# Performance work log

Measured on AMD Instinct MI355X. Metric: run time of the kernel, lower is better.

## Reference

```python
import jax, jax.numpy as jnp
import numpy as np

HEADS = 16
DIM_HEAD = 64
SCALE = DIM_HEAD ** -0.5
NEG = -jnp.finfo(jnp.float32).max


def setup_inputs() -> dict:
    key = jax.random.key(0)
    ks = jax.random.split(key, 5)
    b, n, dim = 2, 2048, 1024
    inner = HEADS * DIM_HEAD
    s = dim ** -0.5  # keep pre-softmax logits well-scaled
    return {
        "x": jax.random.normal(ks[0], (b, n, dim), jnp.float32),
        "mask": jnp.ones((b, n), dtype=bool),
        "Wq": jax.random.normal(ks[1], (dim, inner), jnp.float32) * s,
        "Wk": jax.random.normal(ks[2], (dim, inner), jnp.float32) * s,
        "Wv": jax.random.normal(ks[3], (dim, inner), jnp.float32) * s,
        "Wo": jax.random.normal(ks[4], (inner, dim), jnp.float32) * s,
    }


def reference(x, mask, Wq, Wk, Wv, Wo):
    b, n, _ = x.shape
    # projections, split heads: b n (h d) -> b h n d
    def split(t):
        return t.reshape(b, n, HEADS, DIM_HEAD).transpose(0, 2, 1, 3)
    q = split(x @ Wq)
    k = split(x @ Wk)
    v = split(x @ Wv)
    dots = jnp.einsum("bhid,bhjd->bhij", q, k) * SCALE  # [b,h,n,n]
    # padding mask: b j -> b 1 1 j
    dots = jnp.where(mask[:, None, None, :], dots, NEG)
    # causal mask (strict upper triangle masked)
    causal = jnp.triu(jnp.ones((n, n), dtype=bool), k=1)
    dots = jnp.where(causal, NEG, dots)
    attn = jax.nn.softmax(dots, axis=-1)
    out = jnp.einsum("bhij,bhjd->bhid", attn, v)
    out = out.transpose(0, 2, 1, 3).reshape(b, n, HEADS * DIM_HEAD)
    return out @ Wo
```

## Files before the change

kernel.cpp:

```cpp
#include <hip/hip_runtime.h>
#include <hip/hip_bf16.h>

typedef __bf16 bf16x8 __attribute__((ext_vector_type(8)));
typedef float f32x4 __attribute__((ext_vector_type(4)));
typedef unsigned short u16;
typedef unsigned int u32;

#define MFMA16(A, B, C) __builtin_amdgcn_mfma_f32_16x16x32_bf16((A), (B), (C), 0, 0, 0)

#define BATCH 2
#define SEQ   2048
#define DIM   1024
#define NHEAD 16
#define DHEAD 64
#define MROWS 4096
#define Q_SCALE 0.18033688f

__device__ __forceinline__ u16 f2bf(float f) {
    unsigned int u = __float_as_uint(f);
    u += 0x7fff + ((u >> 16) & 1);
    return (u16)(u >> 16);
}

__device__ __forceinline__ u32 pk2bf(float a, float b) {
    __hip_bfloat162 c = __float22bfloat162_rn(float2{a, b});
    u32 r;
    __builtin_memcpy(&r, &c, 4);
    return r;
}

__device__ __forceinline__ void glds16(const u16* g, u16* l) {
    __builtin_amdgcn_global_load_lds(
        (const __attribute__((address_space(1))) u32*)g,
        (__attribute__((address_space(3))) u32*)l, 16, 0, 0);
}

__global__ __launch_bounds__(256) void prep(const float* __restrict__ x,
                                            const float* __restrict__ wq,
                                            const float* __restrict__ wk,
                                            const float* __restrict__ wv,
                                            const float* __restrict__ wo,
                                            u16* __restrict__ xb,
                                            u16* __restrict__ wt) {
    const int b = blockIdx.x;
    const int t = threadIdx.x;
    if (b < 2048) {
        int i = (b * 256 + t) * 8;
        float4 a = *(const float4*)(x + i);
        float4 c = *(const float4*)(x + i + 4);
        u16 o[8] = {f2bf(a.x), f2bf(a.y), f2bf(a.z), f2bf(a.w),
                    f2bf(c.x), f2bf(c.y), f2bf(c.z), f2bf(c.w)};
        *(uint4*)(xb + i) = *(uint4*)o;
        return;
    }
    __shared__ u16 tile[64][65];
    const int bb = b - 2048;
    const int z = bb >> 8, rem = bb & 255;
    const float* W = (z == 0) ? wq : (z == 1) ? wk : (z == 2) ? wv : wo;
    u16* out = wt + (size_t)z * DIM * DIM;
    int k0 = (rem & 15) * 64;
    int n0 = (rem >> 4) * 64;
    int c = t & 63, r4 = t >> 6;
#pragma unroll
    for (int i = 0; i < 16; i++) {
        int row = i * 4 + r4;
        tile[row][c] = f2bf(W[(size_t)(k0 + row) * DIM + n0 + c]);
    }
    __syncthreads();
#pragma unroll
    for (int i = 0; i < 16; i++) {
        int row = i * 4 + r4;
        out[(size_t)(n0 + row) * DIM + k0 + c] = tile[c][row];
    }
}

__global__ __launch_bounds__(256) void gemm_qkv(const u16* __restrict__ xb,
                                                const u16* __restrict__ wt,
                                                u16* __restrict__ qb,
                                                u16* __restrict__ kb,
                                                u16* __restrict__ vtb) {
    __shared__ __align__(16) u16 SMEM[17408];
    u16* const As = SMEM;
    u16* const Bs = SMEM + 8192;

    const int z = blockIdx.z;
    const u16* Apan = xb;
    const u16* Bpan = wt + (size_t)z * DIM * DIM;
    const int m0 = blockIdx.y * 128, n0 = blockIdx.x * 128;
    const int t = threadIdx.x, w = t >> 6, lane = t & 63;
    const int quad = lane >> 4, l16 = lane & 15;
    const int wm = (w >> 1) * 64, wn = (w & 1) * 64;
    const int srow = lane >> 3;
    const int scol = ((lane & 7) ^ srow) * 8;
    const int fo0 = ((quad) ^ (l16 & 7)) * 8;
    const int fo1 = ((4 + quad) ^ (l16 & 7)) * 8;

    f32x4 acc[4][4] = {};
    for (int k0 = 0; k0 < DIM; k0 += 64) {
        if (k0) __syncthreads();
#pragma unroll
        for (int j = 0; j < 4; j++) {
            int rb = w * 32 + j * 8;
            glds16(Apan + (size_t)(m0 + rb + srow) * DIM + k0 + scol, &As[rb * 64]);
            glds16(Bpan + (size_t)(n0 + rb + srow) * DIM + k0 + scol, &Bs[rb * 64]);
        }
        __syncthreads();

        bf16x8 af[4][2], bfr[4][2];
#pragma unroll
        for (int mt = 0; mt < 4; mt++) {
            const u16* p = &As[(wm + mt * 16 + l16) * 64];
            af[mt][0] = *(const bf16x8*)(p + fo0);
            af[mt][1] = *(const bf16x8*)(p + fo1);
        }
#pragma unroll
        for (int nt = 0; nt < 4; nt++) {
            const u16* p = &Bs[(wn + nt * 16 + l16) * 64];
            bfr[nt][0] = *(const bf16x8*)(p + fo0);
            bfr[nt][1] = *(const bf16x8*)(p + fo1);
        }
#pragma unroll
        for (int mt = 0; mt < 4; mt++)
#pragma unroll
            for (int nt = 0; nt < 4; nt++) {
                acc[mt][nt] = MFMA16(af[mt][0], bfr[nt][0], acc[mt][nt]);
                acc[mt][nt] = MFMA16(af[mt][1], bfr[nt][1], acc[mt][nt]);
            }
    }

    const int bi = m0 >> 11;
    if (z < 2) {
        const float sc = (z == 0) ? Q_SCALE : 1.0f;
        u16* dst = (z == 0) ? qb : kb;
#pragma unroll
        for (int mt = 0; mt < 4; mt++)
#pragma unroll
            for (int nt = 0; nt < 4; nt++)
#pragma unroll
                for (int r = 0; r < 4; r++) {
                    int gm = m0 + wm + mt * 16 + quad * 4 + r;
                    int gc = n0 + wn + nt * 16 + l16;
                    int si = gm & (SEQ - 1);
                    int h = gc >> 6, d = gc & 63;
                    dst[(((size_t)bi * NHEAD + h) * SEQ + si) * DHEAD + d] =
                        f2bf(acc[mt][nt][r] * sc);
                }
    } else {
        __syncthreads();
        u16* T = SMEM;
#pragma unroll
        for (int mt = 0; mt < 4; mt++)
#pragma unroll
            for (int nt = 0; nt < 4; nt++)
#pragma unroll
                for (int r = 0; r < 4; r++)
                    T[(wn + nt * 16 + l16) * 136 + wm + mt * 16 + quad * 4 + r] =
                        f2bf(acc[mt][nt][r]);
        __syncthreads();
        const int row = t >> 1;
        const int half = (t & 1) * 64;
        const int gc = n0 + row;
        const int h = gc >> 6, d = gc & 63;
        const size_t gb = (((size_t)bi * NHEAD + h) * DHEAD + d) * SEQ +
                          (m0 & (SEQ - 1)) + half;
#pragma unroll
        for (int i = 0; i < 8; i++)
            *(uint4*)&vtb[gb + i * 8] = *(const uint4*)&T[row * 136 + half + i * 8];
    }
}

#define LPAD 72
#define OSTR 68
__global__ __launch_bounds__(256) void attn(const u16* __restrict__ qg,
                                            const u16* __restrict__ kg,
                                            const u16* __restrict__ vtg,
                                            u16* __restrict__ og) {
    __shared__ __align__(16) u16 Ks[2][64 * LPAD];
    __shared__ __align__(16) u16 Vs[2][64 * LPAD];
    __shared__ __align__(16) u16 Ps[64 * LPAD];
    float* const Os = (float*)&Ks[0][0];
    float* const Ls = Os + 64 * OSTR;

    const int linear = blockIdx.x;
    const int cls = linear & 7;
    const int inner = linear >> 3;
    const int qt = 31 - (inner >> 2);
    const int bh = cls * 4 + (inner & 3);
    const int t = threadIdx.x, w = t >> 6, lane = t & 63;
    const int quad = lane >> 4, l16 = lane & 15;
    const int wq32 = (w >> 1) * 32, kh = w & 1, kh32 = kh * 32;
    const int srow = t >> 2, sc16 = (t & 3) * 16;
    const size_t qkbase = (size_t)bh * SEQ;
    const size_t vbase = (size_t)bh * DHEAD;
    const int bi = bh >> 4, hh = bh & 15;

    uint4 pk0, pk1, pv0, pv1;
    auto prefetch = [&](int j0) {
        const u16* kp = &kg[(qkbase + j0 + srow) * DHEAD + sc16];
        pk0 = *(const uint4*)kp;
        pk1 = *(const uint4*)(kp + 8);
        const u16* vp = &vtg[(vbase + srow) * SEQ + j0 + sc16];
        pv0 = *(const uint4*)vp;
        pv1 = *(const uint4*)(vp + 8);
    };

    const int q0 = qt * 64;
    const int rowmin = q0 + wq32;

    bf16x8 bq[2][2];
#pragma unroll
    for (int ct = 0; ct < 2; ct++) {
        const u16* qp = qg + (qkbase + q0 + wq32 + ct * 16 + l16) * DHEAD;
        bq[ct][0] = *(const bf16x8*)(qp + quad * 8);
        bq[ct][1] = *(const bf16x8*)(qp + 32 + quad * 8);
    }

    f32x4 accO[4][2] = {};
    float l_part[2] = {0.f, 0.f};

    prefetch(0);

    for (int jt = 0; jt <= qt; jt++) {
        const int buf = jt & 1;
        u16* ksb = &Ks[buf][0];
        u16* vsb = &Vs[buf][0];
        *(uint4*)&ksb[srow * LPAD + sc16] = pk0;
        *(uint4*)&ksb[srow * LPAD + sc16 + 8] = pk1;
        *(uint4*)&vsb[srow * LPAD + sc16] = pv0;
        *(uint4*)&vsb[srow * LPAD + sc16 + 8] = pv1;
        __syncthreads();
        if (jt < qt) prefetch((jt + 1) * 64);

        const int j0 = jt * 64;
        if (j0 + kh32 > rowmin + 31) continue;
        const bool need_mask = (j0 + kh32 + 31 > rowmin);

        bf16x8 ak[2][2];
#pragma unroll
        for (int nt = 0; nt < 2; nt++) {
            const u16* kr = &ksb[(kh32 + nt * 16 + l16) * LPAD];
            ak[nt][0] = *(const bf16x8*)(kr + quad * 8);
            ak[nt][1] = *(const bf16x8*)(kr + 32 + quad * 8);
        }
        f32x4 s[2][2];
#pragma unroll
        for (int nt = 0; nt < 2; nt++)
#pragma unroll
            for (int ct = 0; ct < 2; ct++) {
                f32x4 aa = {};
                aa = MFMA16(ak[nt][0], bq[ct][0], aa);
                aa = MFMA16(ak[nt][1], bq[ct][1], aa);
                s[nt][ct] = aa;
            }

        if (need_mask) {
#pragma unroll
            for (int ct = 0; ct < 2; ct++) {
                int qv = q0 + wq32 + ct * 16 + l16;
#pragma unroll
                for (int nt = 0; nt < 2; nt++) {
                    int kb = j0 + kh32 + nt * 16 + quad * 4;
                    float p[4];
#pragma unroll
                    for (int r = 0; r < 4; r++)
                        p[r] = (kb + r > qv) ? 0.f
                             : __builtin_amdgcn_exp2f(s[nt][ct][r]);
                    l_part[ct] += (p[0] + p[1]) + (p[2] + p[3]);
                    uint2 pkd = {pk2bf(p[0], p[1]), pk2bf(p[2], p[3])};
                    *(uint2*)&Ps[(wq32 + ct * 16 + l16) * LPAD + kh32 +
                                 nt * 16 + quad * 4] = pkd;
                }
            }
        } else {
#pragma unroll
            for (int ct = 0; ct < 2; ct++)
#pragma unroll
                for (int nt = 0; nt < 2; nt++) {
                    float p[4];
#pragma unroll
                    for (int r = 0; r < 4; r++)
                        p[r] = __builtin_amdgcn_exp2f(s[nt][ct][r]);
                    l_part[ct] += (p[0] + p[1]) + (p[2] + p[3]);
                    uint2 pkd = {pk2bf(p[0], p[1]), pk2bf(p[2], p[3])};
                    *(uint2*)&Ps[(wq32 + ct * 16 + l16) * LPAD + kh32 +
                                 nt * 16 + quad * 4] = pkd;
                }
        }

        bf16x8 bp[2];
#pragma unroll
        for (int ct = 0; ct < 2; ct++)
            bp[ct] = *(const bf16x8*)&Ps[(wq32 + ct * 16 + l16) * LPAD +
                                         kh32 + quad * 8];
#pragma unroll
        for (int mt = 0; mt < 4; mt++) {
            bf16x8 av = *(const bf16x8*)&vsb[(mt * 16 + l16) * LPAD +
                                             kh32 + quad * 8];
#pragma unroll
            for (int ct = 0; ct < 2; ct++)
                accO[mt][ct] = MFMA16(av, bp[ct], accO[mt][ct]);
        }
    }

    float l2[2];
#pragma unroll
    for (int ct = 0; ct < 2; ct++) {
        float l = l_part[ct];
        l += __shfl_xor(l, 16);
        l += __shfl_xor(l, 32);
        l2[ct] = l;
    }
    __syncthreads();
    if (kh == 1) {
        if (quad == 0) {
            Ls[wq32 + l16] = l2[0];
            Ls[wq32 + 16 + l16] = l2[1];
        }
#pragma unroll
        for (int mt = 0; mt < 4; mt++)
#pragma unroll
            for (int ct = 0; ct < 2; ct++)
                *(float4*)&Os[(wq32 + ct * 16 + l16) * OSTR + mt * 16 +
                              quad * 4] =
                    float4{accO[mt][ct][0], accO[mt][ct][1],
                           accO[mt][ct][2], accO[mt][ct][3]};
    }
    __syncthreads();
    if (kh == 0) {
#pragma unroll
        for (int ct = 0; ct < 2; ct++) {
            int q = q0 + wq32 + ct * 16 + l16;
            float rl = 1.0f / (l2[ct] + Ls[wq32 + ct * 16 + l16]);
            size_t obase = ((size_t)bi * SEQ + q) * DIM + hh * DHEAD;
#pragma unroll
            for (int mt = 0; mt < 4; mt++) {
                float4 o = *(float4*)&Os[(wq32 + ct * 16 + l16) * OSTR +
                                         mt * 16 + quad * 4];
                float v0 = (accO[mt][ct][0] + o.x) * rl;
                float v1 = (accO[mt][ct][1] + o.y) * rl;
                float v2 = (accO[mt][ct][2] + o.z) * rl;
                float v3 = (accO[mt][ct][3] + o.w) * rl;
                uint2 pkd = {pk2bf(v0, v1), pk2bf(v2, v3)};
                *(uint2*)&og[obase + mt * 16 + quad * 4] = pkd;
            }
        }
    }
}

__global__ __launch_bounds__(256) void gemm_out(const u16* __restrict__ ob,
                                                const u16* __restrict__ wot,
                                                float* __restrict__ out) {
    __shared__ __align__(16) u16 As[64 * 64];
    __shared__ __align__(16) u16 Bs[128 * 64];
    const int m0 = blockIdx.y * 64, n0 = blockIdx.x * 128;
    const int t = threadIdx.x, w = t >> 6, lane = t & 63;
    const int quad = lane >> 4, l16 = lane & 15;
    const int wm = (w >> 1) * 32, wn = (w & 1) * 64;
    const int srow = lane >> 3;
    const int scol = ((lane & 7) ^ srow) * 8;
    const int fo0 = ((quad) ^ (l16 & 7)) * 8;
    const int fo1 = ((4 + quad) ^ (l16 & 7)) * 8;

    f32x4 acc[2][4] = {};
    for (int k0 = 0; k0 < DIM; k0 += 64) {
        if (k0) __syncthreads();
#pragma unroll
        for (int j = 0; j < 2; j++) {
            int rb = w * 16 + j * 8;
            glds16(&ob[(size_t)(m0 + rb + srow) * DIM + k0 + scol], &As[rb * 64]);
        }
#pragma unroll
        for (int j = 0; j < 4; j++) {
            int rb = w * 32 + j * 8;
            glds16(&wot[(size_t)(n0 + rb + srow) * DIM + k0 + scol], &Bs[rb * 64]);
        }
        __syncthreads();

        bf16x8 af[2][2], bfr[4][2];
#pragma unroll
        for (int mt = 0; mt < 2; mt++) {
            const u16* p = &As[(wm + mt * 16 + l16) * 64];
            af[mt][0] = *(const bf16x8*)(p + fo0);
            af[mt][1] = *(const bf16x8*)(p + fo1);
        }
#pragma unroll
        for (int nt = 0; nt < 4; nt++) {
            const u16* p = &Bs[(wn + nt * 16 + l16) * 64];
            bfr[nt][0] = *(const bf16x8*)(p + fo0);
            bfr[nt][1] = *(const bf16x8*)(p + fo1);
        }
#pragma unroll
        for (int mt = 0; mt < 2; mt++)
#pragma unroll
            for (int nt = 0; nt < 4; nt++) {
                acc[mt][nt] = MFMA16(af[mt][0], bfr[nt][0], acc[mt][nt]);
                acc[mt][nt] = MFMA16(af[mt][1], bfr[nt][1], acc[mt][nt]);
            }
    }
#pragma unroll
    for (int mt = 0; mt < 2; mt++)
#pragma unroll
        for (int nt = 0; nt < 4; nt++)
#pragma unroll
            for (int r = 0; r < 4; r++) {
                int gm = m0 + wm + mt * 16 + quad * 4 + r;
                int gc = n0 + wn + nt * 16 + l16;
                out[(size_t)gm * DIM + gc] = acc[mt][nt][r];
            }
}

extern "C" void kernel_launch(void* const* d_in, const int* in_sizes, int n_in,
                              void* d_out, int out_size, void* d_ws, size_t ws_size,
                              hipStream_t stream) {
    const float* x  = (const float*)d_in[0];
    const float* wq = (const float*)d_in[2];
    const float* wk = (const float*)d_in[3];
    const float* wv = (const float*)d_in[4];
    const float* wo = (const float*)d_in[5];
    float* out = (float*)d_out;

    char* ws = (char*)d_ws;
    u16* xb  = (u16*)(ws);
    u16* wt  = (u16*)(ws + (8ull  << 20));
    u16* qb  = (u16*)(ws + (16ull << 20));
    u16* kb  = (u16*)(ws + (24ull << 20));
    u16* vtb = (u16*)(ws + (32ull << 20));
    u16* obf = (u16*)(ws + (40ull << 20));

    prep<<<3072, 256, 0, stream>>>(x, wq, wk, wv, wo, xb, wt);
    gemm_qkv<<<dim3(DIM / 128, MROWS / 128, 3), 256, 0, stream>>>(xb, wt, qb, kb, vtb);
    attn<<<1024, 256, 0, stream>>>(qb, kb, vtb, obf);
    gemm_out<<<dim3(DIM / 128, MROWS / 64), 256, 0, stream>>>(
        obf, wt + 3ull * DIM * DIM, out);
}
```

Baseline: 172.1 us.

## Enlarge attention query tile to 128 rows with 512 threads and swizzled LDS

The attention kernel now processes 128 query rows per block with 8 waves instead of 64 rows with 4 waves, halving the grid and sharing each loaded K/V tile across more query rows. LDS padding is replaced by an XOR swizzle on the K, V and P tiles to avoid bank conflicts in a smaller footprint, and s_setprio is raised around the MFMA sections to favour matrix issue. Larger blocks cut redundant K/V loads but lengthen per-block causal work and may reduce occupancy and load balance.

```diff
diff --git a/kernel.cpp b/kernel.cpp
--- a/kernel.cpp
+++ b/kernel.cpp
@@ -169,43 +169,42 @@
     }
 }
 
-#define LPAD 72
 #define OSTR 68
-__global__ __launch_bounds__(256) void attn(const u16* __restrict__ qg,
+__global__ __launch_bounds__(512) void attn(const u16* __restrict__ qg,
                                             const u16* __restrict__ kg,
                                             const u16* __restrict__ vtg,
                                             u16* __restrict__ og) {
-    __shared__ __align__(16) u16 Ks[2][64 * LPAD];
-    __shared__ __align__(16) u16 Vs[2][64 * LPAD];
-    __shared__ __align__(16) u16 Ps[64 * LPAD];
-    float* const Os = (float*)&Ks[0][0];
-    float* const Ls = Os + 64 * OSTR;
+    __shared__ __align__(16) u16 SMEM[24576];
+    float* const Os = (float*)SMEM;
+    float* const Ls = Os + 128 * OSTR;
 
     const int linear = blockIdx.x;
     const int cls = linear & 7;
     const int inner = linear >> 3;
-    const int qt = 31 - (inner >> 2);
+    const int qt = 15 - (inner >> 2);
     const int bh = cls * 4 + (inner & 3);
     const int t = threadIdx.x, w = t >> 6, lane = t & 63;
     const int quad = lane >> 4, l16 = lane & 15;
     const int wq32 = (w >> 1) * 32, kh = w & 1, kh32 = kh * 32;
-    const int srow = t >> 2, sc16 = (t & 3) * 16;
+    const int sr = t >> 3, sg = t & 7;
+    const int soff = sr * 64 + ((sg ^ (sr & 7)) * 8);
     const size_t qkbase = (size_t)bh * SEQ;
     const size_t vbase = (size_t)bh * DHEAD;
     const int bi = bh >> 4, hh = bh & 15;
 
-    uint4 pk0, pk1, pv0, pv1;
+    uint4 pk, pv;
     auto prefetch = [&](int j0) {
-        const u16* kp = &kg[(qkbase + j0 + srow) * DHEAD + sc16];
-        pk0 = *(const uint4*)kp;
-        pk1 = *(const uint4*)(kp + 8);
-        const u16* vp = &vtg[(vbase + srow) * SEQ + j0 + sc16];
-        pv0 = *(const uint4*)vp;
-        pv1 = *(const uint4*)(vp + 8);
+        pk = *(const uint4*)&kg[(qkbase + j0 + sr) * DHEAD + sg * 8];
+        pv = *(const uint4*)&vtg[(vbase + sr) * SEQ + j0 + sg * 8];
     };
 
-    const int q0 = qt * 64;
+    const int q0 = qt * 128;
     const int rowmin = q0 + wq32;
+    const int nit = 2 * qt + 2;
+
+    const int fo0 = ((quad) ^ (l16 & 7)) * 8;
+    const int fo1 = ((4 + quad) ^ (l16 & 7)) * 8;
+    const int vo = (((kh << 2) + quad) ^ (l16 & 7)) * 8;
 
     bf16x8 bq[2][2];
 #pragma unroll
@@ -220,16 +219,15 @@
 
     prefetch(0);
 
-    for (int jt = 0; jt <= qt; jt++) {
+    for (int jt = 0; jt < nit; jt++) {
         const int buf = jt & 1;
-        u16* ksb = &Ks[buf][0];
-        u16* vsb = &Vs[buf][0];
-        *(uint4*)&ksb[srow * LPAD + sc16] = pk0;
-        *(uint4*)&ksb[srow * LPAD + sc16 + 8] = pk1;
-        *(uint4*)&vsb[srow * LPAD + sc16] = pv0;
-        *(uint4*)&vsb[srow * LPAD + sc16 + 8] = pv1;
+        u16* ksb = &SMEM[buf * 4096];
+        u16* vsb = &SMEM[8192 + buf * 4096];
+        u16* Ps = &SMEM[16384];
+        *(uint4*)&ksb[soff] = pk;
+        *(uint4*)&vsb[soff] = pv;
         __syncthreads();
-        if (jt < qt) prefetch((jt + 1) * 64);
+        if (jt + 1 < nit) prefetch((jt + 1) * 64);
 
         const int j0 = jt * 64;
         if (j0 + kh32 > rowmin + 31) continue;
@@ -238,11 +236,12 @@
         bf16x8 ak[2][2];
 #pragma unroll
         for (int nt = 0; nt < 2; nt++) {
-            const u16* kr = &ksb[(kh32 + nt * 16 + l16) * LPAD];
-            ak[nt][0] = *(const bf16x8*)(kr + quad * 8);
-            ak[nt][1] = *(const bf16x8*)(kr + 32 + quad * 8);
+            const u16* kr = &ksb[(kh32 + nt * 16 + l16) * 64];
+            ak[nt][0] = *(const bf16x8*)(kr + fo0);
+            ak[nt][1] = *(const bf16x8*)(kr + fo1);
         }
         f32x4 s[2][2];
+        __builtin_amdgcn_s_setprio(1);
 #pragma unroll
         for (int nt = 0; nt < 2; nt++)
 #pragma unroll
@@ -252,54 +251,48 @@
                 aa = MFMA16(ak[nt][1], bq[ct][1], aa);
                 s[nt][ct] = aa;
             }
-
-        if (need_mask) {
-#pragma unroll
-            for (int ct = 0; ct < 2; ct++) {
-                int qv = q0 + wq32 + ct * 16 + l16;
-#pragma unroll
-                for (int nt = 0; nt < 2; nt++) {
+        __builtin_amdgcn_s_setprio(0);
+
+#pragma unroll
+        for (int ct = 0; ct < 2; ct++) {
+            const int row = wq32 + ct * 16 + l16;
+            const int qv = q0 + row;
+            u16* const prow = &Ps[row * 64];
+            const int rx = (row & 7);
+#pragma unroll
+            for (int nt = 0; nt < 2; nt++) {
+                float p[4];
+                if (need_mask) {
                     int kb = j0 + kh32 + nt * 16 + quad * 4;
-                    float p[4];
 #pragma unroll
                     for (int r = 0; r < 4; r++)
                         p[r] = (kb + r > qv) ? 0.f
                              : __builtin_amdgcn_exp2f(s[nt][ct][r]);
-                    l_part[ct] += (p[0] + p[1]) + (p[2] + p[3]);
-                    uint2 pkd = {pk2bf(p[0], p[1]), pk2bf(p[2], p[3])};
-                    *(uint2*)&Ps[(wq32 + ct * 16 + l16) * LPAD + kh32 +
-                                 nt * 16 + quad * 4] = pkd;
-                }
-            }
-        } else {
-#pragma unroll
-            for (int ct = 0; ct < 2; ct++)
-#pragma unroll
-                for (int nt = 0; nt < 2; nt++) {
-                    float p[4];
+                } else {
 #pragma unroll
                     for (int r = 0; r < 4; r++)
                         p[r] = __builtin_amdgcn_exp2f(s[nt][ct][r]);
-                    l_part[ct] += (p[0] + p[1]) + (p[2] + p[3]);
-                    uint2 pkd = {pk2bf(p[0], p[1]), pk2bf(p[2], p[3])};
-                    *(uint2*)&Ps[(wq32 + ct * 16 + l16) * LPAD + kh32 +
-                                 nt * 16 + quad * 4] = pkd;
                 }
+                l_part[ct] += (p[0] + p[1]) + (p[2] + p[3]);
+                uint2 pkd = {pk2bf(p[0], p[1]), pk2bf(p[2], p[3])};
+                int G = (kh << 2) + nt * 2 + (quad >> 1);
+                *(uint2*)&prow[((G ^ rx) * 8) + (quad & 1) * 4] = pkd;
+            }
         }
 
         bf16x8 bp[2];
 #pragma unroll
         for (int ct = 0; ct < 2; ct++)
-            bp[ct] = *(const bf16x8*)&Ps[(wq32 + ct * 16 + l16) * LPAD +
-                                         kh32 + quad * 8];
+            bp[ct] = *(const bf16x8*)&Ps[(wq32 + ct * 16 + l16) * 64 + vo];
+        __builtin_amdgcn_s_setprio(1);
 #pragma unroll
         for (int mt = 0; mt < 4; mt++) {
-            bf16x8 av = *(const bf16x8*)&vsb[(mt * 16 + l16) * LPAD +
-                                             kh32 + quad * 8];
+            bf16x8 av = *(const bf16x8*)&vsb[(mt * 16 + l16) * 64 + vo];
 #pragma unroll
             for (int ct = 0; ct < 2; ct++)
                 accO[mt][ct] = MFMA16(av, bp[ct], accO[mt][ct]);
         }
+        __builtin_amdgcn_s_setprio(0);
     }
 
     float l2[2];
@@ -429,7 +422,7 @@
 
     prep<<<3072, 256, 0, stream>>>(x, wq, wk, wv, wo, xb, wt);
     gemm_qkv<<<dim3(DIM / 128, MROWS / 128, 3), 256, 0, stream>>>(xb, wt, qb, kb, vtb);
-    attn<<<1024, 256, 0, stream>>>(qb, kb, vtb, obf);
+    attn<<<512, 512, 0, stream>>>(qb, kb, vtb, obf);
     gemm_out<<<dim3(DIM / 128, MROWS / 64), 256, 0, stream>>>(
         obf, wt + 3ull * DIM * DIM, out);
 }
```

New measurement: 168.4 us. -2.1%, faster.

## Enlarge attention query tile to 128 rows with per-wave P buffers

Applied to the files above, without the earlier changes.

The attention kernel now processes 128 query rows per block instead of 64. Each wave pair handles a 64-row strip, so every K/V tile loaded into shared memory is reused across twice as many queries and the grid halves to 512 blocks. P is staged in per-wave private shared buffers, and s_setprio is raised around the MFMA sections. The cost is more registers per thread (accO grows to 4x4 tiles), fewer blocks to balance across CUs, and a coarser causal-skip granularity.

```diff
diff --git a/kernel.cpp b/kernel.cpp
--- a/kernel.cpp
+++ b/kernel.cpp
@@ -171,24 +171,24 @@
 
 #define LPAD 72
 #define OSTR 68
+#define PSTR 40
 __global__ __launch_bounds__(256) void attn(const u16* __restrict__ qg,
                                             const u16* __restrict__ kg,
                                             const u16* __restrict__ vtg,
                                             u16* __restrict__ og) {
-    __shared__ __align__(16) u16 Ks[2][64 * LPAD];
-    __shared__ __align__(16) u16 Vs[2][64 * LPAD];
-    __shared__ __align__(16) u16 Ps[64 * LPAD];
-    float* const Os = (float*)&Ks[0][0];
-    float* const Ls = Os + 64 * OSTR;
+    __shared__ __align__(16) u16 SMEM[28672];
+    float* const Os = (float*)SMEM;
+    float* const Ls = Os + 128 * OSTR;
 
     const int linear = blockIdx.x;
     const int cls = linear & 7;
     const int inner = linear >> 3;
-    const int qt = 31 - (inner >> 2);
+    const int qt = 15 - (inner >> 2);
     const int bh = cls * 4 + (inner & 3);
     const int t = threadIdx.x, w = t >> 6, lane = t & 63;
     const int quad = lane >> 4, l16 = lane & 15;
-    const int wq32 = (w >> 1) * 32, kh = w & 1, kh32 = kh * 32;
+    const int strip = (w >> 1) * 64;
+    const int kh = w & 1, kh32 = kh * 32;
     const int srow = t >> 2, sc16 = (t & 3) * 16;
     const size_t qkbase = (size_t)bh * SEQ;
     const size_t vbase = (size_t)bh * DHEAD;
@@ -204,35 +204,38 @@
         pv1 = *(const uint4*)(vp + 8);
     };
 
-    const int q0 = qt * 64;
-    const int rowmin = q0 + wq32;
-
-    bf16x8 bq[2][2];
-#pragma unroll
-    for (int ct = 0; ct < 2; ct++) {
-        const u16* qp = qg + (qkbase + q0 + wq32 + ct * 16 + l16) * DHEAD;
+    const int q0 = qt * 128;
+    const int rowmin = q0 + strip;
+    const int nit = 2 * qt + 2;
+
+    u16* const Pw = SMEM + 18432 + w * 2560;
+
+    bf16x8 bq[4][2];
+#pragma unroll
+    for (int ct = 0; ct < 4; ct++) {
+        const u16* qp = qg + (qkbase + q0 + strip + ct * 16 + l16) * DHEAD;
         bq[ct][0] = *(const bf16x8*)(qp + quad * 8);
         bq[ct][1] = *(const bf16x8*)(qp + 32 + quad * 8);
     }
 
-    f32x4 accO[4][2] = {};
-    float l_part[2] = {0.f, 0.f};
+    f32x4 accO[4][4] = {};
+    float l_part[4] = {0.f, 0.f, 0.f, 0.f};
 
     prefetch(0);
 
-    for (int jt = 0; jt <= qt; jt++) {
+    for (int jt = 0; jt < nit; jt++) {
         const int buf = jt & 1;
-        u16* ksb = &Ks[buf][0];
-        u16* vsb = &Vs[buf][0];
+        u16* ksb = &SMEM[buf * 4608];
+        u16* vsb = &SMEM[9216 + buf * 4608];
         *(uint4*)&ksb[srow * LPAD + sc16] = pk0;
         *(uint4*)&ksb[srow * LPAD + sc16 + 8] = pk1;
         *(uint4*)&vsb[srow * LPAD + sc16] = pv0;
         *(uint4*)&vsb[srow * LPAD + sc16 + 8] = pv1;
         __syncthreads();
-        if (jt < qt) prefetch((jt + 1) * 64);
+        if (jt + 1 < nit) prefetch((jt + 1) * 64);
 
         const int j0 = jt * 64;
-        if (j0 + kh32 > rowmin + 31) continue;
+        if (j0 + kh32 > rowmin + 63) continue;
         const bool need_mask = (j0 + kh32 + 31 > rowmin);
 
         bf16x8 ak[2][2];
@@ -242,69 +245,63 @@
             ak[nt][0] = *(const bf16x8*)(kr + quad * 8);
             ak[nt][1] = *(const bf16x8*)(kr + 32 + quad * 8);
         }
-        f32x4 s[2][2];
+        f32x4 s[2][4];
+        __builtin_amdgcn_s_setprio(1);
 #pragma unroll
         for (int nt = 0; nt < 2; nt++)
 #pragma unroll
-            for (int ct = 0; ct < 2; ct++) {
+            for (int ct = 0; ct < 4; ct++) {
                 f32x4 aa = {};
                 aa = MFMA16(ak[nt][0], bq[ct][0], aa);
                 aa = MFMA16(ak[nt][1], bq[ct][1], aa);
                 s[nt][ct] = aa;
             }
-
-        if (need_mask) {
-#pragma unroll
-            for (int ct = 0; ct < 2; ct++) {
-                int qv = q0 + wq32 + ct * 16 + l16;
-#pragma unroll
-                for (int nt = 0; nt < 2; nt++) {
+        __builtin_amdgcn_s_setprio(0);
+
+#pragma unroll
+        for (int ct = 0; ct < 4; ct++) {
+            const int row = ct * 16 + l16;
+            const int qv = q0 + strip + row;
+            u16* const prow = &Pw[row * PSTR];
+#pragma unroll
+            for (int nt = 0; nt < 2; nt++) {
+                float p[4];
+                if (need_mask) {
                     int kb = j0 + kh32 + nt * 16 + quad * 4;
-                    float p[4];
 #pragma unroll
                     for (int r = 0; r < 4; r++)
                         p[r] = (kb + r > qv) ? 0.f
                              : __builtin_amdgcn_exp2f(s[nt][ct][r]);
-                    l_part[ct] += (p[0] + p[1]) + (p[2] + p[3]);
-                    uint2 pkd = {pk2bf(p[0], p[1]), pk2bf(p[2], p[3])};
-                    *(uint2*)&Ps[(wq32 + ct * 16 + l16) * LPAD + kh32 +
-                                 nt * 16 + quad * 4] = pkd;
-                }
-            }
-        } else {
-#pragma unroll
-            for (int ct = 0; ct < 2; ct++)
-#pragma unroll
-                for (int nt = 0; nt < 2; nt++) {
-                    float p[4];
+                } else {
 #pragma unroll
                     for (int r = 0; r < 4; r++)
                         p[r] = __builtin_amdgcn_exp2f(s[nt][ct][r]);
-                    l_part[ct] += (p[0] + p[1]) + (p[2] + p[3]);
-                    uint2 pkd = {pk2bf(p[0], p[1]), pk2bf(p[2], p[3])};
-                    *(uint2*)&Ps[(wq32 + ct * 16 + l16) * LPAD + kh32 +
-                                 nt * 16 + quad * 4] = pkd;
                 }
-        }
-
-        bf16x8 bp[2];
-#pragma unroll
-        for (int ct = 0; ct < 2; ct++)
-            bp[ct] = *(const bf16x8*)&Ps[(wq32 + ct * 16 + l16) * LPAD +
-                                         kh32 + quad * 8];
+                l_part[ct] += (p[0] + p[1]) + (p[2] + p[3]);
+                uint2 pkd = {pk2bf(p[0], p[1]), pk2bf(p[2], p[3])};
+                *(uint2*)&prow[nt * 16 + quad * 4] = pkd;
+            }
+        }
+
+        bf16x8 bp[4];
+#pragma unroll
+        for (int ct = 0; ct < 4; ct++)
+            bp[ct] = *(const bf16x8*)&Pw[(ct * 16 + l16) * PSTR + quad * 8];
+        __builtin_amdgcn_s_setprio(1);
 #pragma unroll
         for (int mt = 0; mt < 4; mt++) {
             bf16x8 av = *(const bf16x8*)&vsb[(mt * 16 + l16) * LPAD +
                                              kh32 + quad * 8];
 #pragma unroll
-            for (int ct = 0; ct < 2; ct++)
+            for (int ct = 0; ct < 4; ct++)
                 accO[mt][ct] = MFMA16(av, bp[ct], accO[mt][ct]);
         }
-    }
-
-    float l2[2];
-#pragma unroll
-    for (int ct = 0; ct < 2; ct++) {
+        __builtin_amdgcn_s_setprio(0);
+    }
+
+    float l2[4];
+#pragma unroll
+    for (int ct = 0; ct < 4; ct++) {
         float l = l_part[ct];
         l += __shfl_xor(l, 16);
         l += __shfl_xor(l, 32);
@@ -313,14 +310,15 @@
     __syncthreads();
     if (kh == 1) {
         if (quad == 0) {
-            Ls[wq32 + l16] = l2[0];
-            Ls[wq32 + 16 + l16] = l2[1];
+#pragma unroll
+            for (int ct = 0; ct < 4; ct++)
+                Ls[strip + ct * 16 + l16] = l2[ct];
         }
 #pragma unroll
         for (int mt = 0; mt < 4; mt++)
 #pragma unroll
-            for (int ct = 0; ct < 2; ct++)
-                *(float4*)&Os[(wq32 + ct * 16 + l16) * OSTR + mt * 16 +
+            for (int ct = 0; ct < 4; ct++)
+                *(float4*)&Os[(strip + ct * 16 + l16) * OSTR + mt * 16 +
                               quad * 4] =
                     float4{accO[mt][ct][0], accO[mt][ct][1],
                            accO[mt][ct][2], accO[mt][ct][3]};
@@ -328,13 +326,13 @@
     __syncthreads();
     if (kh == 0) {
 #pragma unroll
-        for (int ct = 0; ct < 2; ct++) {
-            int q = q0 + wq32 + ct * 16 + l16;
-            float rl = 1.0f / (l2[ct] + Ls[wq32 + ct * 16 + l16]);
+        for (int ct = 0; ct < 4; ct++) {
+            int q = q0 + strip + ct * 16 + l16;
+            float rl = 1.0f / (l2[ct] + Ls[strip + ct * 16 + l16]);
             size_t obase = ((size_t)bi * SEQ + q) * DIM + hh * DHEAD;
 #pragma unroll
             for (int mt = 0; mt < 4; mt++) {
-                float4 o = *(float4*)&Os[(wq32 + ct * 16 + l16) * OSTR +
+                float4 o = *(float4*)&Os[(strip + ct * 16 + l16) * OSTR +
                                          mt * 16 + quad * 4];
                 float v0 = (accO[mt][ct][0] + o.x) * rl;
                 float v1 = (accO[mt][ct][1] + o.y) * rl;
@@ -429,7 +427,7 @@
 
     prep<<<3072, 256, 0, stream>>>(x, wq, wk, wv, wo, xb, wt);
     gemm_qkv<<<dim3(DIM / 128, MROWS / 128, 3), 256, 0, stream>>>(xb, wt, qb, kb, vtb);
-    attn<<<1024, 256, 0, stream>>>(qb, kb, vtb, obf);
+    attn<<<512, 256, 0, stream>>>(qb, kb, vtb, obf);
     gemm_out<<<dim3(DIM / 128, MROWS / 64), 256, 0, stream>>>(
         obf, wt + 3ull * DIM * DIM, out);
 }
```

Result: slower. 189.3 us (+10.0%).
